# Performance work log

Hardware: AMD Instinct MI355X
Metric: run time of the kernel (lower is better)

Reference implementation:

```python
import jax, jax.numpy as jnp
import numpy as np

HIDDEN = 50


def setup_inputs() -> dict:
    key = jax.random.key(0)
    k1, k2, k3, k4, k5 = jax.random.split(key, 5)
    B, S, H = 1024, 2048, HIDDEN
    scale = 1.0 / np.sqrt(H)
    return {
        "decoder_prev_state": jax.random.normal(k1, (B, H), dtype=jnp.float32),
        "encoder_states": jax.random.normal(k2, (S, B, H), dtype=jnp.float32),
        "mask": jnp.ones((B, S), dtype=jnp.int32),
        "W_prev": jax.random.uniform(k3, (H, H), jnp.float32, -scale, scale),
        "W_enc": jax.random.uniform(k4, (H, H), jnp.float32, -scale, scale),
        "W_score": jax.random.uniform(k5, (1, H), jnp.float32, -scale, scale),
    }


def reference(decoder_prev_state, encoder_states, mask, W_prev, W_enc, W_score):
    # encoder_states: (S, B, H) -> (B, S, H)
    enc = jnp.transpose(encoder_states, (1, 0, 2))
    proj_prev = decoder_prev_state @ W_prev.T          # (B, H)
    proj_enc = enc @ W_enc.T                           # (B, S, H)
    tanh_out = jnp.tanh(proj_prev[:, None, :] + proj_enc)  # (B, S, H)
    scores = jnp.einsum("bsh,h->bs", tanh_out, W_score[0])  # (B, S)
    scores = jnp.where(mask == 0, -jnp.inf, scores)
    attn = jax.nn.softmax(scores, axis=-1)             # (B, S)
    # context: (B, H) = sum_s enc[b,s,:] * attn[b,s]
    context = jnp.einsum("bsh,bs->bh", enc, attn)
    return context
```

## Files before the change

kernel.cpp:

```cpp
#include <hip/hip_runtime.h>

#define H 50
#define B_TOT 1024
#define S_TOT 2048

static __device__ __forceinline__ float fast_rcp(float x) {
#if __has_builtin(__builtin_amdgcn_rcpf)
    return __builtin_amdgcn_rcpf(x);
#else
    return 1.0f / x;
#endif
}

static __device__ __forceinline__ float fast_tanh(float x) {
    return fmaf(-2.0f, fast_rcp(__expf(2.0f * x) + 1.0f), 1.0f);
}

__global__ __launch_bounds__(256) void pp_kernel(const float* __restrict__ dps,
                                                 const float* __restrict__ Wp,
                                                 float* __restrict__ pp) {
    int tid = blockIdx.x * 256 + threadIdx.x;
    int b = tid / H, j = tid - b * H;
    const float* dr = dps + b * H;
    const float* wr = Wp + j * H;
    float a0 = 0.f, a1 = 0.f, a2 = 0.f, a3 = 0.f;
#pragma unroll
    for (int k = 0; k < 48; k += 4) {
        a0 = fmaf(dr[k + 0], wr[k + 0], a0);
        a1 = fmaf(dr[k + 1], wr[k + 1], a1);
        a2 = fmaf(dr[k + 2], wr[k + 2], a2);
        a3 = fmaf(dr[k + 3], wr[k + 3], a3);
    }
    a0 = fmaf(dr[48], wr[48], a0);
    a1 = fmaf(dr[49], wr[49], a1);
    pp[tid] = (a0 + a1) + (a2 + a3);
}

__global__ __launch_bounds__(256, 2) void attn_main(const float* __restrict__ enc,
                                                    const int* __restrict__ mask,
                                                    const float* __restrict__ Wenc,
                                                    const float* __restrict__ Wsc,
                                                    const float* __restrict__ pp,
                                                    float* __restrict__ pl,
                                                    float* __restrict__ pctx,
                                                    int SC) {
    const int c = blockIdx.x;
    const int b = blockIdx.y * 256 + threadIdx.x;
    const int s0 = c * SC;

    float ctx[H];
#pragma unroll
    for (int h = 0; h < H; ++h) ctx[h] = 0.f;
    float lsum = 0.f;

    float ppr[H];
    {
        const float* pr = pp + b * H;
#pragma unroll
        for (int j = 0; j < H; j += 2) {
            float2 v = *reinterpret_cast<const float2*>(pr + j);
            ppr[j] = v.x;
            ppr[j + 1] = v.y;
        }
    }

    const int* mrow = mask + (size_t)b * S_TOT;

    for (int si = 0; si < SC; ++si) {
        const int s = s0 + si;
        const float* er = enc + ((size_t)s * B_TOT + b) * H;

        float e[H];
#pragma unroll
        for (int q = 0; q < H; q += 2) {
            float2 v = *reinterpret_cast<const float2*>(er + q);
            e[q] = v.x;
            e[q + 1] = v.y;
        }

        float score = 0.f;
        for (int j = 0; j < H; ++j) {
            const float* wr = Wenc + j * H;
            float a0 = ppr[j], a1 = 0.f, a2 = 0.f, a3 = 0.f;
#pragma unroll
            for (int k = 0; k < 48; k += 4) {
                a0 = fmaf(wr[k + 0], e[k + 0], a0);
                a1 = fmaf(wr[k + 1], e[k + 1], a1);
                a2 = fmaf(wr[k + 2], e[k + 2], a2);
                a3 = fmaf(wr[k + 3], e[k + 3], a3);
            }
            a0 = fmaf(wr[48], e[48], a0);
            a1 = fmaf(wr[49], e[49], a1);
            float acc = (a0 + a1) + (a2 + a3);
            score = fmaf(fast_tanh(acc), Wsc[j], score);
        }

        const float p = (mrow[s] != 0) ? __expf(score) : 0.0f;
        lsum += p;
#pragma unroll
        for (int h = 0; h < H; ++h) ctx[h] = fmaf(p, e[h], ctx[h]);
    }

    pl[c * B_TOT + b] = lsum;
    float* po = pctx + ((size_t)c * B_TOT + b) * H;
#pragma unroll
    for (int h = 0; h < H; ++h) po[h] = ctx[h];
}

__global__ __launch_bounds__(256) void combine_kernel(const float* __restrict__ pl,
                                                      const float* __restrict__ pctx,
                                                      float* __restrict__ out,
                                                      int NC) {
    int tid = blockIdx.x * 256 + threadIdx.x;
    int b = tid / H;
    float csum = 0.f, lsum = 0.f;
    for (int c = 0; c < NC; ++c) {
        csum += pctx[(size_t)c * (B_TOT * H) + tid];
        lsum += pl[c * B_TOT + b];
    }
    out[tid] = csum / lsum;
}

extern "C" void kernel_launch(void* const* d_in, const int* in_sizes, int n_in,
                              void* d_out, int out_size, void* d_ws, size_t ws_size,
                              hipStream_t stream) {
    const float* dps  = (const float*)d_in[0];
    const float* enc  = (const float*)d_in[1];
    const int*   mask = (const int*)d_in[2];
    const float* Wp   = (const float*)d_in[3];
    const float* We   = (const float*)d_in[4];
    const float* Wsc  = (const float*)d_in[5];
    float* out = (float*)d_out;
    float* ws  = (float*)d_ws;

    int NC = 256;
    while (NC > 1 &&
           (size_t)(B_TOT * H + (size_t)NC * B_TOT * (H + 1)) * sizeof(float) > ws_size)
        NC >>= 1;
    const int SC = S_TOT / NC;

    float* pp   = ws;
    float* pl   = ws + B_TOT * H;
    float* pctx = pl + (size_t)NC * B_TOT;

    hipLaunchKernelGGL(pp_kernel, dim3((B_TOT * H) / 256), dim3(256), 0, stream,
                       dps, Wp, pp);
    hipLaunchKernelGGL(attn_main, dim3(NC, B_TOT / 256), dim3(256), 0, stream,
                       enc, mask, We, Wsc, pp, pl, pctx, SC);
    hipLaunchKernelGGL(combine_kernel, dim3((B_TOT * H) / 256), dim3(256), 0, stream,
                       pl, pctx, out, NC);
}
```

Baseline: 849.5 us.

## Stage encoder rows through LDS and restructure projection as outer-product accumulation

Each block now copies its 256 encoder rows for one sequence step into shared memory with coalesced float4 loads, replacing the strided per-thread float2 loads. The projection is reorganized as an outer product over a transposed W_enc, built by a new small kernel, with 25 accumulators per pass, so each weight element is a uniform scalar load and no longer needs a per-output dot-product reduction. The occupancy hint rises to 3 blocks per SIMD. The cost is 50 KB of LDS per block and two barriers per sequence step, which may limit occupancy and serialize load and compute.

```diff
diff --git a/kernel.cpp b/kernel.cpp
--- a/kernel.cpp
+++ b/kernel.cpp
@@ -3,6 +3,8 @@
 #define H 50
 #define B_TOT 1024
 #define S_TOT 2048
+
+typedef float f4 __attribute__((ext_vector_type(4)));
 
 static __device__ __forceinline__ float fast_rcp(float x) {
 #if __has_builtin(__builtin_amdgcn_rcpf)
@@ -36,75 +38,103 @@
     pp[tid] = (a0 + a1) + (a2 + a3);
 }
 
-__global__ __launch_bounds__(256, 2) void attn_main(const float* __restrict__ enc,
+__global__ __launch_bounds__(256) void wet_kernel(const float* __restrict__ We,
+                                                  float* __restrict__ WeT) {
+    int id = blockIdx.x * 256 + threadIdx.x;
+    if (id < H * H) {
+        int k = id / H, j = id - k * H;
+        WeT[id] = We[j * H + k];
+    }
+}
+
+__global__ __launch_bounds__(256, 3) void attn_main(const float* __restrict__ enc,
                                                     const int* __restrict__ mask,
-                                                    const float* __restrict__ Wenc,
+                                                    const float* __restrict__ WeT,
                                                     const float* __restrict__ Wsc,
                                                     const float* __restrict__ pp,
                                                     float* __restrict__ pl,
                                                     float* __restrict__ pctx,
                                                     int SC) {
-    const int c = blockIdx.x;
-    const int b = blockIdx.y * 256 + threadIdx.x;
-    const int s0 = c * SC;
+    __shared__ float tile[256 * H];
+    const int tid = threadIdx.x;
+    const int b0 = blockIdx.y * 256;
+    const int b = b0 + tid;
+    const int s0 = blockIdx.x * SC;
+
+    {
+        const f4* src = reinterpret_cast<const f4*>(pp + (size_t)b0 * H);
+        f4* dst = reinterpret_cast<f4*>(tile);
+#pragma unroll
+        for (int r = 0; r < 12; ++r) dst[r * 256 + tid] = src[r * 256 + tid];
+        if (tid < 128) dst[3072 + tid] = src[3072 + tid];
+    }
+    __syncthreads();
+    float ppr[H];
+#pragma unroll
+    for (int q = 0; q < H; q += 2) {
+        float2 v = *reinterpret_cast<const float2*>(&tile[tid * H + q]);
+        ppr[q] = v.x;
+        ppr[q + 1] = v.y;
+    }
+    __syncthreads();
 
     float ctx[H];
 #pragma unroll
     for (int h = 0; h < H; ++h) ctx[h] = 0.f;
     float lsum = 0.f;
 
-    float ppr[H];
-    {
-        const float* pr = pp + b * H;
-#pragma unroll
-        for (int j = 0; j < H; j += 2) {
-            float2 v = *reinterpret_cast<const float2*>(pr + j);
-            ppr[j] = v.x;
-            ppr[j + 1] = v.y;
-        }
-    }
-
     const int* mrow = mask + (size_t)b * S_TOT;
 
+#pragma unroll 1
     for (int si = 0; si < SC; ++si) {
         const int s = s0 + si;
-        const float* er = enc + ((size_t)s * B_TOT + b) * H;
+        {
+            const f4* src =
+                reinterpret_cast<const f4*>(enc + ((size_t)s * B_TOT + b0) * H);
+            f4* dst = reinterpret_cast<f4*>(tile);
+#pragma unroll
+            for (int r = 0; r < 12; ++r) dst[r * 256 + tid] = src[r * 256 + tid];
+            if (tid < 128) dst[3072 + tid] = src[3072 + tid];
+        }
+        __syncthreads();
 
-        float e[H];
+        const float* erow = &tile[tid * H];
+        float score = 0.f;
 #pragma unroll
-        for (int q = 0; q < H; q += 2) {
-            float2 v = *reinterpret_cast<const float2*>(er + q);
-            e[q] = v.x;
-            e[q + 1] = v.y;
-        }
-
-        float score = 0.f;
-        for (int j = 0; j < H; ++j) {
-            const float* wr = Wenc + j * H;
-            float a0 = ppr[j], a1 = 0.f, a2 = 0.f, a3 = 0.f;
+        for (int pass = 0; pass < 2; ++pass) {
+            float acc[25];
 #pragma unroll
-            for (int k = 0; k < 48; k += 4) {
-                a0 = fmaf(wr[k + 0], e[k + 0], a0);
-                a1 = fmaf(wr[k + 1], e[k + 1], a1);
-                a2 = fmaf(wr[k + 2], e[k + 2], a2);
-                a3 = fmaf(wr[k + 3], e[k + 3], a3);
+            for (int jj = 0; jj < 25; ++jj) acc[jj] = ppr[pass * 25 + jj];
+#pragma unroll
+            for (int k = 0; k < H; k += 2) {
+                float2 e2 = *reinterpret_cast<const float2*>(erow + k);
+                const float* w0 = WeT + k * H + pass * 25;
+                const float* w1 = WeT + (k + 1) * H + pass * 25;
+#pragma unroll
+                for (int jj = 0; jj < 25; ++jj) acc[jj] = fmaf(e2.x, w0[jj], acc[jj]);
+#pragma unroll
+                for (int jj = 0; jj < 25; ++jj) acc[jj] = fmaf(e2.y, w1[jj], acc[jj]);
             }
-            a0 = fmaf(wr[48], e[48], a0);
-            a1 = fmaf(wr[49], e[49], a1);
-            float acc = (a0 + a1) + (a2 + a3);
-            score = fmaf(fast_tanh(acc), Wsc[j], score);
+#pragma unroll
+            for (int jj = 0; jj < 25; ++jj)
+                score = fmaf(fast_tanh(acc[jj]), Wsc[pass * 25 + jj], score);
         }
 
         const float p = (mrow[s] != 0) ? __expf(score) : 0.0f;
         lsum += p;
 #pragma unroll
-        for (int h = 0; h < H; ++h) ctx[h] = fmaf(p, e[h], ctx[h]);
+        for (int q = 0; q < H; q += 2) {
+            float2 e2 = *reinterpret_cast<const float2*>(erow + q);
+            ctx[q] = fmaf(p, e2.x, ctx[q]);
+            ctx[q + 1] = fmaf(p, e2.y, ctx[q + 1]);
+        }
+        __syncthreads();
     }
 
-    pl[c * B_TOT + b] = lsum;
-    float* po = pctx + ((size_t)c * B_TOT + b) * H;
+    pl[blockIdx.x * B_TOT + b] = lsum;
+    float* po = pctx + ((size_t)blockIdx.x * B_TOT + b) * H;
 #pragma unroll
-    for (int h = 0; h < H; ++h) po[h] = ctx[h];
+    for (int q = 0; q < H; ++q) po[q] = ctx[q];
 }
 
 __global__ __launch_bounds__(256) void combine_kernel(const float* __restrict__ pl,
@@ -135,18 +165,22 @@
 
     int NC = 256;
     while (NC > 1 &&
-           (size_t)(B_TOT * H + (size_t)NC * B_TOT * (H + 1)) * sizeof(float) > ws_size)
+           (size_t)(B_TOT * H + (size_t)NC * B_TOT * (H + 1) + H * H) * sizeof(float) >
+               ws_size)
         NC >>= 1;
     const int SC = S_TOT / NC;
 
     float* pp   = ws;
     float* pl   = ws + B_TOT * H;
     float* pctx = pl + (size_t)NC * B_TOT;
+    float* WeT  = pctx + (size_t)NC * B_TOT * H;
 
     hipLaunchKernelGGL(pp_kernel, dim3((B_TOT * H) / 256), dim3(256), 0, stream,
                        dps, Wp, pp);
+    hipLaunchKernelGGL(wet_kernel, dim3((H * H + 255) / 256), dim3(256), 0, stream,
+                       We, WeT);
     hipLaunchKernelGGL(attn_main, dim3(NC, B_TOT / 256), dim3(256), 0, stream,
-                       enc, mask, We, Wsc, pp, pl, pctx, SC);
+                       enc, mask, WeT, Wsc, pp, pl, pctx, SC);
     hipLaunchKernelGGL(combine_kernel, dim3((B_TOT * H) / 256), dim3(256), 0, stream,
                        pl, pctx, out, NC);
 }
```

After: 1.261 ms. 48.5% more time.
